# Kernel tuning notes

Measured on AMD Instinct MI355X. Metric: run time of the kernel, lower is better.

Reference implementation:

```python
import math
import jax, jax.numpy as jnp
import numpy as np

# hyperparameters (module defaults; w_scale overridden to 1.0)
EMA_SPEED = 0.05
REW_SENS = 1.0
LR = 0.0033
MOMENTUM = 0.4
UNTANH = 0.6
SPEED = 0.5
WIDTH = 0.1
WD = 0.01
LAT_DECAY = 0.01
NOISE_SCALE = 0.8
C_MOMENT = 0.99
W_SCALE = 1.0


def rms_norm(x, axis=-1):
    return x * jax.lax.rsqrt(jnp.mean(x * x, axis=axis, keepdims=True) + 1e-6)


def setup_inputs() -> dict:
    key = jax.random.key(0)
    ks = jax.random.split(key, 16)
    B, N, D = 16, 128, 64
    s = 1.0 / math.sqrt(D)
    return {
        'eye_env': jax.random.normal(ks[0], (B, D), jnp.float32),
        'stomach_env': jax.random.normal(ks[1], (B, D), jnp.float32),
        'state': jax.random.normal(ks[2], (B, N, D), jnp.float32),
        'output': jax.random.normal(ks[3], (B, N, D), jnp.float32),
        'W1': jax.random.normal(ks[4], (B, N, D, D), jnp.float32) * s,
        'W2': jax.random.normal(ks[5], (B, N, D, D), jnp.float32) * s,
        'W3': jax.random.normal(ks[6], (B, N, D, D), jnp.float32) * s,
        'M1': jax.random.normal(ks[7], (B, N, D, D), jnp.float32) * 0.2,
        'M2': jax.random.normal(ks[8], (B, N, D, D), jnp.float32) * 0.2,
        'M3': jax.random.normal(ks[9], (B, N, D, D), jnp.float32) * 0.2,
        'E_baseline': jax.random.uniform(ks[10], (B, N, D), jnp.float32),
        'A': jax.nn.softmax(jax.random.normal(ks[11], (B, N, N), jnp.float32), axis=2),
        'noise_A': jax.random.normal(ks[12], (B, N, N), jnp.float32),
        'noise1_raw': jax.random.normal(ks[13], (B, N, D), jnp.float32),
        'noise2_raw': jax.random.normal(ks[14], (B, N, D), jnp.float32),
        'step_counter': 0,
    }


def reference(eye_env, stomach_env, state, output, W1, W2, W3, M1, M2, M3,
              E_baseline, A, noise_A, noise1_raw, noise2_raw, step_counter):
    B, N, D = state.shape
    sc = jnp.float32(step_counter) + 1.0  # self.step_counter += 1

    # attention routing
    q = jnp.einsum('bnj,bnjk->bnk', state, W3)
    k = jnp.einsum('bnj,bnjk->bnk', state, W2)
    raw_A = jnp.einsum('bnd,bmd->bnm', q, k) / math.sqrt(D) + noise_A * 1e-5
    P_dense = jax.nn.softmax(raw_A, axis=2)
    keep = (P_dense > 1.0 / (N + 1.0)) | (P_dense == jnp.max(P_dense, axis=2, keepdims=True))
    P = jax.nn.softmax(jnp.where(keep, raw_A, -jnp.inf), axis=2)
    A_new = A * C_MOMENT + P * (1.0 - C_MOMENT)
    A_new = A_new.at[:, 0:2, :].set(0.0)

    # message passing + sensory clamp
    target = jnp.einsum('bnm,bmd->bnd', A_new, output)
    target = target.at[:, 0].set(eye_env).at[:, 1].set(stomach_env)

    # prediction
    raw_pred = jnp.einsum('bnj,bnjk->bnk', state, W1)
    raw = raw_pred - jnp.tanh(raw_pred) * UNTANH
    prediction = jnp.tanh(raw) * math.sqrt(2.0 + math.sqrt(2.0))

    err = prediction - target
    E_curr = jax.nn.softmax(err, axis=-1)
    bmask = (E_baseline == 0).astype(jnp.float32)
    Eb = E_baseline * (1.0 - bmask) + E_curr * bmask
    Eb = Eb * (1.0 - EMA_SPEED) + EMA_SPEED * E_curr
    advantage = E_curr - Eb
    R = -rms_norm(advantage[..., None] * REW_SENS)  # (B,N,D,1)
    mask = (Eb > 0).astype(jnp.float32)[..., None]

    # noise injection
    state_mag = jnp.sum(jnp.abs(state), axis=(-2, -1), keepdims=True)
    noise1 = noise1_raw / (1.0 + state_mag)
    noise2 = noise2_raw * jnp.std(err, ddof=1) * NOISE_SCALE
    noisy_state = state + noise1 + noise2

    # Hebbian outer-product gradient, G_NORM=1.0 -> rms-normalized
    lg = -jnp.einsum('bni,bnj->bnij', err, noisy_state)
    lg = rms_norm(lg, axis=(2, 3))

    plasticity = 1.0 - R
    grad1 = plasticity * lg * mask + LAT_DECAY * W3 - WD * W1
    grad2 = plasticity * lg * mask + LAT_DECAY * W1 - WD * W2
    grad3 = plasticity * lg * mask + LAT_DECAY * W2 - WD * W3

    # travelling gaussian column mask
    idx = jnp.arange(D, dtype=jnp.float32).reshape(1, 1, 1, D)
    center = (sc * SPEED) % D
    diff = jnp.abs(idx - center)
    diff = jnp.minimum(diff, D - diff)
    g_mask = jnp.exp(-diff ** 2 / (2.0 * WIDTH ** 2 + 1e-6))

    M1n = M1 * MOMENTUM + (1.0 - MOMENTUM) * (grad1 * g_mask)
    M2n = M2 * MOMENTUM + (1.0 - MOMENTUM) * (grad2 * g_mask)
    M3n = M3 * MOMENTUM + (1.0 - MOMENTUM) * (grad3 * g_mask)
    W1n = rms_norm(W1 + LR * M1n) * W_SCALE
    W2n = rms_norm(W2 + LR * M2n) * W_SCALE
    W3n = rms_norm(W3 + LR * M3n) * W_SCALE

    # new output = prediction, new state = target
    return prediction, target, A_new, W1n, W2n, W3n
```

## Files before the change

kernel.cpp:

```cpp
#include <hip/hip_runtime.h>
#include <hip/hip_bf16.h>

typedef __hip_bfloat16 bf16;
typedef float f32x4 __attribute__((ext_vector_type(4)));

__device__ __forceinline__ float b2f(bf16 x) { return __bfloat162float(x); }

template<bool F32>
__device__ __forceinline__ float ld(const void* p, size_t i) {
  if constexpr (F32) return ((const float*)p)[i];
  else return b2f(((const bf16*)p)[i]);
}

template<bool F32>
__device__ __forceinline__ void ld4(const void* p, size_t i, float v[4]) {
  if constexpr (F32) {
    const float4 a = *(const float4*)((const float*)p + i);
    v[0]=a.x; v[1]=a.y; v[2]=a.z; v[3]=a.w;
  } else {
    union { uint2 u; bf16 h[4]; } t;
    t.u = *(const uint2*)((const bf16*)p + i);
    #pragma unroll
    for (int c = 0; c < 4; ++c) v[c] = b2f(t.h[c]);
  }
}

template<bool F32>
__device__ __forceinline__ void ld8(const void* p, size_t i, float v[8]) {
  if constexpr (F32) {
    const float4 a = *(const float4*)((const float*)p + i);
    const float4 b = *(const float4*)((const float*)p + i + 4);
    v[0]=a.x; v[1]=a.y; v[2]=a.z; v[3]=a.w;
    v[4]=b.x; v[5]=b.y; v[6]=b.z; v[7]=b.w;
  } else {
    union { uint4 u; bf16 h[8]; } t;
    t.u = *(const uint4*)((const bf16*)p + i);
    #pragma unroll
    for (int c = 0; c < 8; ++c) v[c] = b2f(t.h[c]);
  }
}

template<bool F32>
__device__ __forceinline__ void ld8nt(const void* p, size_t i, float v[8]) {
  if constexpr (F32) {
    const f32x4* q = (const f32x4*)((const float*)p + i);
    const f32x4 a = __builtin_nontemporal_load(q);
    const f32x4 b = __builtin_nontemporal_load(q + 1);
    v[0]=a[0]; v[1]=a[1]; v[2]=a[2]; v[3]=a[3];
    v[4]=b[0]; v[5]=b[1]; v[6]=b[2]; v[7]=b[3];
  } else {
    ld8<false>(p, i, v);
  }
}

__device__ __forceinline__ float plast(float Ec, float Ebl) {
  const float Eb0 = (Ebl == 0.f) ? Ec : Ebl;
  const float Eb  = Eb0 * 0.95f + 0.05f * Ec;
  const float adv = Ec - Eb;
  const float R   = -adv * rsqrtf(adv*adv + 1e-6f);
  return (Eb > 0.f) ? (1.f - R) : 0.f;
}


template<bool F32>
__device__ __forceinline__ void k1_wave(
    const void* state, const void* W1, const void* W2, const void* W3,
    float* qw, float* kw, float* magn, float* out_pred,
    int node, int mat, int lane)
{
  const float st = ld<F32>(state, (size_t)node*64 + lane);
  const int jg = lane >> 4, cq = lane & 15;
  const int c0 = cq * 4;
  const size_t nb = (size_t)node*4096 + (size_t)jg*1024 + c0;
  const void* W = (mat == 0) ? W3 : (mat == 1) ? W2 : W1;

  float acc[4] = {0.f, 0.f, 0.f, 0.f};
  float buf[8][4];
  #pragma unroll
  for (int jj = 0; jj < 8; ++jj) ld4<F32>(W, nb + (size_t)jj*64, buf[jj]);
  #pragma unroll
  for (int jj = 0; jj < 8; ++jj) {
    const float sj = __shfl(st, jg*16 + jj, 64);
    #pragma unroll
    for (int cc = 0; cc < 4; ++cc) acc[cc] += sj * buf[jj][cc];
  }
  #pragma unroll
  for (int jj = 0; jj < 8; ++jj) ld4<F32>(W, nb + (size_t)(jj + 8)*64, buf[jj]);
  #pragma unroll
  for (int jj = 0; jj < 8; ++jj) {
    const float sj = __shfl(st, jg*16 + 8 + jj, 64);
    #pragma unroll
    for (int cc = 0; cc < 4; ++cc) acc[cc] += sj * buf[jj][cc];
  }
  #pragma unroll
  for (int cc = 0; cc < 4; ++cc) {
    acc[cc] += __shfl_xor(acc[cc], 16, 64);
    acc[cc] += __shfl_xor(acc[cc], 32, 64);
  }

  if (mat == 2) {
    float am = fabsf(st);
    #pragma unroll
    for (int s = 32; s; s >>= 1) am += __shfl_xor(am, s, 64);
    if (lane == 0) magn[node] = am;
    if (jg == 0) {
      float pr[4];
      #pragma unroll
      for (int cc = 0; cc < 4; ++cc) {
        const float raw = acc[cc] - tanhf(acc[cc]) * 0.6f;
        pr[cc] = tanhf(raw) * 1.8477590650225735f;
      }
      *(float4*)(out_pred + (size_t)node*64 + c0) = make_float4(pr[0], pr[1], pr[2], pr[3]);
    }
  } else if (jg == 0) {
    float* dst = (mat == 0) ? qw : kw;
    *(float4*)(dst + (size_t)node*64 + c0) = make_float4(acc[0], acc[1], acc[2], acc[3]);
  }
}

__global__ __launch_bounds__(256) void k1_qkpred(
    const void* __restrict__ state,
    const void* __restrict__ W1, const void* __restrict__ W2,
    const void* __restrict__ W3,
    float* __restrict__ qw, float* __restrict__ kw,
    float* __restrict__ magn, float* __restrict__ out_pred,
    int* __restrict__ flagws, float* __restrict__ stats)
{
  const int tid = threadIdx.x;
  const int w = tid >> 6, lane = tid & 63;
  bool huge = false;
  for (int i = lane; i < 1024; i += 64) {
    const float x = b2f(((const bf16*)state)[i]);
    if (!(fabsf(x) < 1e5f)) huge = true;
  }
  const bool f32 = (__ballot(huge) != 0ull);
  if (blockIdx.x == 0 && tid == 0) {
    *flagws = f32 ? 1 : 0;
    stats[0] = 0.f; stats[1] = 0.f;
  }
  const int wid = blockIdx.x * 4 + w;
  const int node = wid & 2047, mat = wid >> 11;
  if (f32) k1_wave<true >(state, W1, W2, W3, qw, kw, magn, out_pred, node, mat, lane);
  else     k1_wave<false>(state, W1, W2, W3, qw, kw, magn, out_pred, node, mat, lane);
}

template<bool F32>
__device__ __forceinline__ void k2_body(
    const float* qw, const float* kw, const float* predw,
    const void* noiseA, const void* Aold, const void* outp,
    const void* eye, const void* stomach, const void* Ebase,
    const float* magn, float* mag,
    float* errw, float* plw, float* stats,
    float* out_target, float* out_A,
    float* s_k, float* s_q, float* s_A)
{
  const int bidx = blockIdx.x;
  const int b = bidx >> 4;
  const int n0 = (bidx & 15) * 8;
  const int tid = threadIdx.x;

  if (n0 == 0 && tid < 64) {
    float v = magn[b*128 + tid] + magn[b*128 + 64 + tid];
    #pragma unroll
    for (int s = 32; s; s >>= 1) v += __shfl_xor(v, s, 64);
    if (tid == 0) mag[b] = v;
  }

  {
    const float* kwb = kw + (size_t)b * 8192;
    #pragma unroll
    for (int it = 0; it < 8; ++it) {
      const int idx = it*256 + tid;
      const int m = idx >> 4, dq = idx & 15;
      const float4 v = *(const float4*)(kwb + (size_t)idx * 4);
      float* dst = &s_k[m*65 + dq*4];
      dst[0] = v.x; dst[1] = v.y; dst[2] = v.z; dst[3] = v.w;
    }
    if (tid < 128) {
      const int rr = tid >> 4, dq = tid & 15;
      *(float4*)&s_q[rr*64 + dq*4] =
          *(const float4*)(qw + ((size_t)(b*128 + n0 + rr))*64 + dq*4);
    }
  }
  __syncthreads();

  const int rr = tid >> 5, c = tid & 31;
  const int n = n0 + rr;
  const size_t node = (size_t)b*128 + n;

  float acc[4] = {0.f, 0.f, 0.f, 0.f};
  {
    const float* qrow = s_q + rr*64;
    #pragma unroll 8
    for (int j = 0; j < 64; ++j) {
      const float qv = qrow[j];
      acc[0] += qv * s_k[(c     )*65 + j];
      acc[1] += qv * s_k[(c + 32)*65 + j];
      acc[2] += qv * s_k[(c + 64)*65 + j];
      acc[3] += qv * s_k[(c + 96)*65 + j];
    }
  }
  float raw[4];
  #pragma unroll
  for (int i = 0; i < 4; ++i)
    raw[i] = acc[i]*0.125f + 1e-5f*ld<F32>(noiseA, node*128 + c + 32*i);

  float rmx = fmaxf(fmaxf(raw[0], raw[1]), fmaxf(raw[2], raw[3]));
  #pragma unroll
  for (int s = 16; s >= 1; s >>= 1) rmx = fmaxf(rmx, __shfl_xor(rmx, s, 64));
  float e[4], S = 0.f;
  #pragma unroll
  for (int i = 0; i < 4; ++i) { e[i] = expf(raw[i] - rmx); S += e[i]; }
  #pragma unroll
  for (int s = 16; s >= 1; s >>= 1) S += __shfl_xor(S, s, 64);
  float ek[4], Sk = 0.f;
  #pragma unroll
  for (int i = 0; i < 4; ++i) {
    const float Pd = e[i] / S;
    ek[i] = ((Pd > 0.007751937984496124f) || (raw[i] == rmx)) ? e[i] : 0.f;
    Sk += ek[i];
  }
  #pragma unroll
  for (int s = 16; s >= 1; s >>= 1) Sk += __shfl_xor(Sk, s, 64);
  #pragma unroll
  for (int i = 0; i < 4; ++i) {
    const int m = c + 32*i;
    const float P = ek[i] / Sk;
    const float An = (n < 2) ? 0.f
                   : 0.99f * ld<F32>(Aold, node*128 + m) + 0.01f * P;
    out_A[node*128 + m] = An;
    s_A[rr*128 + m] = An;
  }
  __syncthreads();

  float t0, t1;
  if (n == 0) {
    t0 = ld<F32>(eye, (size_t)b*64 + c);
    t1 = ld<F32>(eye, (size_t)b*64 + c + 32);
  } else if (n == 1) {
    t0 = ld<F32>(stomach, (size_t)b*64 + c);
    t1 = ld<F32>(stomach, (size_t)b*64 + c + 32);
  } else {
    t0 = 0.f; t1 = 0.f;
    const float* arow = s_A + rr*128;
    const size_t ob = (size_t)b * 8192;
    #pragma unroll 4
    for (int m = 0; m < 128; ++m) {
      const float a = arow[m];
      t0 += a * ld<F32>(outp, ob + m*64 + c);
      t1 += a * ld<F32>(outp, ob + m*64 + c + 32);
    }
  }
  out_target[node*64 + c]      = t0;
  out_target[node*64 + c + 32] = t1;
  const float e0 = predw[node*64 + c]      - t0;
  const float e1 = predw[node*64 + c + 32] - t1;
  errw[node*64 + c]      = e0;
  errw[node*64 + c + 32] = e1;

  float mx = fmaxf(e0, e1);
  #pragma unroll
  for (int s = 16; s >= 1; s >>= 1) mx = fmaxf(mx, __shfl_xor(mx, s, 64));
  const float x0 = expf(e0 - mx), x1 = expf(e1 - mx);
  float ss = x0 + x1;
  #pragma unroll
  for (int s = 16; s >= 1; s >>= 1) ss += __shfl_xor(ss, s, 64);
  plw[node*64 + c]      = plast(x0/ss, ld<F32>(Ebase, node*64 + c));
  plw[node*64 + c + 32] = plast(x1/ss, ld<F32>(Ebase, node*64 + c + 32));

  float se = e0 + e1, sq = e0*e0 + e1*e1;
  #pragma unroll
  for (int s = 16; s >= 1; s >>= 1) { se += __shfl_xor(se, s, 64); sq += __shfl_xor(sq, s, 64); }
  if (c == 0) { atomicAdd(&stats[0], se); atomicAdd(&stats[1], sq); }
}

__global__ __launch_bounds__(256) void k2_attn(
    const int* __restrict__ flag,
    const float* __restrict__ qw, const float* __restrict__ kw,
    const float* __restrict__ predw,
    const void* __restrict__ noiseA, const void* __restrict__ Aold,
    const void* __restrict__ outp,
    const void* __restrict__ eye, const void* __restrict__ stomach,
    const void* __restrict__ Ebase,
    const float* __restrict__ magn, float* __restrict__ mag,
    float* __restrict__ errw, float* __restrict__ plw,
    float* __restrict__ stats,
    float* __restrict__ out_target, float* __restrict__ out_A)
{
  __shared__ alignas(16) float s_k[128*65];
  __shared__ alignas(16) float s_q[8*64];
  __shared__ alignas(16) float s_A[8*128];
  if (*flag) k2_body<true >(qw,kw,predw,noiseA,Aold,outp,eye,stomach,Ebase,magn,mag,errw,plw,stats,out_target,out_A,s_k,s_q,s_A);
  else       k2_body<false>(qw,kw,predw,noiseA,Aold,outp,eye,stomach,Ebase,magn,mag,errw,plw,stats,out_target,out_A,s_k,s_q,s_A);
}

template<bool F32>
__device__ __forceinline__ void k3_body(
    const float* errw, const float* plw,
    const void* state, const void* n1raw, const void* n2raw,
    const float* mag, const float* stats, const int* stepc,
    const void* W1, const void* W2, const void* W3,
    const void* M1, const void* M2, const void* M3,
    float* oW1, float* oW2, float* oW3)
{
  const int node = blockIdx.x;
  const int b = node >> 7;
  const int tid = threadIdx.x;
  const int lane = tid & 63;
  const int r = tid >> 3;
  const int l8 = tid & 7;

  const size_t sb = (size_t)node*64 + lane;
  const float e_i  = errw[sb];
  const float pl_i = plw[sb];
  const float st_i = ld<F32>(state, sb);
  const float n1_i = ld<F32>(n1raw, sb);
  const float n2_i = ld<F32>(n2raw, sb);
  const float magb = mag[b];
  const float S1 = stats[0], S2 = stats[1];
  const float scv = (float)stepc[0] + 1.f;

  const size_t off = (size_t)node*4096 + (size_t)r*64 + (size_t)l8*8;
  float w1v[8], w2v[8], w3v[8], m1v[8], m2v[8], m3v[8];
  ld8  <F32>(W1, off, w1v); ld8  <F32>(W2, off, w2v); ld8  <F32>(W3, off, w3v);
  ld8nt<F32>(M1, off, m1v); ld8nt<F32>(M2, off, m2v); ld8nt<F32>(M3, off, m3v);

  const float Mn = 131072.f;
  const float var = (S2 - S1*S1/Mn) / (Mn - 1.f);
  const float stdv = sqrtf(fmaxf(var, 0.f));
  const float ns_i = st_i + n1_i / (1.f + magb)
                   + n2_i * stdv * 0.8f;
  float e2 = e_i*e_i, q2 = ns_i*ns_i;
  #pragma unroll
  for (int s = 32; s; s >>= 1) { e2 += __shfl_xor(e2, s, 64); q2 += __shfl_xor(q2, s, 64); }
  const float c_i  = -ns_i * rsqrtf(e2 * q2 * (1.f/4096.f) + 1e-6f);
  const float pe_i = pl_i * e_i;
  const float center = fmodf(scv * 0.5f, 64.f);
  float dff = fabsf((float)lane - center);
  dff = fminf(dff, 64.f - dff);
  const float g_i = expf(-dff*dff * (1.f/0.020001f));

  const float pe = __shfl(pe_i, r, 64);
  float cj[8], gj[8];
  #pragma unroll
  for (int cc = 0; cc < 8; ++cc) {
    const int j = l8*8 + cc;
    cj[cc] = __shfl(c_i, j, 64);
    gj[cc] = __shfl(g_i, j, 64);
  }

  float t1[8], t2[8], t3[8];
  float ss1 = 0.f, ss2 = 0.f, ss3 = 0.f;
  #pragma unroll
  for (int cc = 0; cc < 8; ++cc) {
    const float lgterm = pe * cj[cc];
    const float g = gj[cc];
    const float g1 = lgterm + 0.01f*w3v[cc] - 0.01f*w1v[cc];
    const float g2 = lgterm + 0.01f*w1v[cc] - 0.01f*w2v[cc];
    const float g3 = lgterm + 0.01f*w2v[cc] - 0.01f*w3v[cc];
    const float v1 = w1v[cc] + 0.0033f*(0.4f*m1v[cc] + 0.6f*g1*g);
    const float v2 = w2v[cc] + 0.0033f*(0.4f*m2v[cc] + 0.6f*g2*g);
    const float v3 = w3v[cc] + 0.0033f*(0.4f*m3v[cc] + 0.6f*g3*g);
    t1[cc] = v1; t2[cc] = v2; t3[cc] = v3;
    ss1 += v1*v1; ss2 += v2*v2; ss3 += v3*v3;
  }
  #pragma unroll
  for (int s = 1; s <= 4; s <<= 1) {
    ss1 += __shfl_xor(ss1, s, 64);
    ss2 += __shfl_xor(ss2, s, 64);
    ss3 += __shfl_xor(ss3, s, 64);
  }
  const float r1 = rsqrtf(ss1*(1.f/64.f) + 1e-6f);
  const float r2 = rsqrtf(ss2*(1.f/64.f) + 1e-6f);
  const float r3 = rsqrtf(ss3*(1.f/64.f) + 1e-6f);
  *(float4*)(oW1 + off)     = make_float4(t1[0]*r1, t1[1]*r1, t1[2]*r1, t1[3]*r1);
  *(float4*)(oW1 + off + 4) = make_float4(t1[4]*r1, t1[5]*r1, t1[6]*r1, t1[7]*r1);
  *(float4*)(oW2 + off)     = make_float4(t2[0]*r2, t2[1]*r2, t2[2]*r2, t2[3]*r2);
  *(float4*)(oW2 + off + 4) = make_float4(t2[4]*r2, t2[5]*r2, t2[6]*r2, t2[7]*r2);
  *(float4*)(oW3 + off)     = make_float4(t3[0]*r3, t3[1]*r3, t3[2]*r3, t3[3]*r3);
  *(float4*)(oW3 + off + 4) = make_float4(t3[4]*r3, t3[5]*r3, t3[6]*r3, t3[7]*r3);
}

__global__ __launch_bounds__(512) void k3_update(
    const int* __restrict__ flag,
    const float* __restrict__ errw, const float* __restrict__ plw,
    const void* __restrict__ state, const void* __restrict__ n1raw,
    const void* __restrict__ n2raw,
    const float* __restrict__ mag, const float* __restrict__ stats,
    const int* __restrict__ stepc,
    const void* __restrict__ W1, const void* __restrict__ W2,
    const void* __restrict__ W3,
    const void* __restrict__ M1, const void* __restrict__ M2,
    const void* __restrict__ M3,
    float* __restrict__ oW1, float* __restrict__ oW2, float* __restrict__ oW3)
{
  if (*flag) k3_body<true >(errw,plw,state,n1raw,n2raw,mag,stats,stepc,W1,W2,W3,M1,M2,M3,oW1,oW2,oW3);
  else       k3_body<false>(errw,plw,state,n1raw,n2raw,mag,stats,stepc,W1,W2,W3,M1,M2,M3,oW1,oW2,oW3);
}

extern "C" void kernel_launch(void* const* d_in, const int* in_sizes, int n_in,
                              void* d_out, int out_size, void* d_ws, size_t ws_size,
                              hipStream_t stream) {
  const void* eye     = d_in[0];
  const void* stomach = d_in[1];
  const void* state   = d_in[2];
  const void* outp    = d_in[3];
  const void* W1      = d_in[4];
  const void* W2      = d_in[5];
  const void* W3      = d_in[6];
  const void* M1      = d_in[7];
  const void* M2      = d_in[8];
  const void* M3      = d_in[9];
  const void* Ebase   = d_in[10];
  const void* Aold    = d_in[11];
  const void* noiseA  = d_in[12];
  const void* n1raw   = d_in[13];
  const void* n2raw   = d_in[14];
  const int*  stepc   = (const int*)d_in[15];

  float* ws    = (float*)d_ws;
  float* qw    = ws;
  float* kw    = ws + 131072;
  float* errw  = ws + 262144;
  float* plw   = ws + 393216;
  float* magn  = ws + 524288;
  float* mag   = ws + 526336;
  float* stats = ws + 526352;
  int*   flag  = (int*)(ws + 526354);

  float* out        = (float*)d_out;
  float* out_pred   = out;
  float* out_target = out + 131072;
  float* out_A      = out + 262144;
  float* oW1        = out + 524288;
  float* oW2        = out + 8912896;
  float* oW3        = out + 17301504;

  k1_qkpred<<<1536, 256, 0, stream>>>(state, W1, W2, W3, qw, kw, magn, out_pred,
                                      flag, stats);
  k2_attn<<<256, 256, 0, stream>>>(flag, qw, kw, out_pred, noiseA, Aold, outp,
                                   eye, stomach, Ebase, magn, mag, errw, plw, stats,
                                   out_target, out_A);
  k3_update<<<2048, 512, 0, stream>>>(flag, errw, plw, state, n1raw, n2raw, mag, stats,
                                      stepc, W1, W2, W3, M1, M2, M3, oW1, oW2, oW3);
}
```

Measured before the change: 333.3 us.

## Remap attention kernel to one wave per row and issue all weight loads at once

The attention kernel now assigns one 64-lane wave per query row, with 4 rows per block and twice as many blocks, instead of 8 rows split across half-waves. Each row's softmax and target reductions stay inside a single wave, and the block-wide barrier between computing A and the target matvec is removed. The goal is more parallelism and less synchronisation in this small kernel. The cost is that each block reloads the full K matrix into shared memory, so that staging traffic doubles. Separately, the k1 weight matvec loads all 16 float4 weight rows before any accumulation, instead of two batches of 8, to put more loads in flight at the expense of extra registers.

```diff
diff --git a/kernel.cpp b/kernel.cpp
--- a/kernel.cpp
+++ b/kernel.cpp
@@ -75,20 +75,12 @@
   const void* W = (mat == 0) ? W3 : (mat == 1) ? W2 : W1;
 
   float acc[4] = {0.f, 0.f, 0.f, 0.f};
-  float buf[8][4];
-  #pragma unroll
-  for (int jj = 0; jj < 8; ++jj) ld4<F32>(W, nb + (size_t)jj*64, buf[jj]);
-  #pragma unroll
-  for (int jj = 0; jj < 8; ++jj) {
+  float buf[16][4];
+  #pragma unroll
+  for (int jj = 0; jj < 16; ++jj) ld4<F32>(W, nb + (size_t)jj*64, buf[jj]);
+  #pragma unroll
+  for (int jj = 0; jj < 16; ++jj) {
     const float sj = __shfl(st, jg*16 + jj, 64);
-    #pragma unroll
-    for (int cc = 0; cc < 4; ++cc) acc[cc] += sj * buf[jj][cc];
-  }
-  #pragma unroll
-  for (int jj = 0; jj < 8; ++jj) ld4<F32>(W, nb + (size_t)(jj + 8)*64, buf[jj]);
-  #pragma unroll
-  for (int jj = 0; jj < 8; ++jj) {
-    const float sj = __shfl(st, jg*16 + 8 + jj, 64);
     #pragma unroll
     for (int cc = 0; cc < 4; ++cc) acc[cc] += sj * buf[jj][cc];
   }
@@ -155,11 +147,12 @@
     float* s_k, float* s_q, float* s_A)
 {
   const int bidx = blockIdx.x;
-  const int b = bidx >> 4;
-  const int n0 = (bidx & 15) * 8;
+  const int b = bidx >> 5;
+  const int n0 = (bidx & 31) * 4;
   const int tid = threadIdx.x;
-
-  if (n0 == 0 && tid < 64) {
+  const int w = tid >> 6, lane = tid & 63;
+
+  if ((bidx & 31) == 0 && tid < 64) {
     float v = magn[b*128 + tid] + magn[b*128 + 64 + tid];
     #pragma unroll
     for (int s = 32; s; s >>= 1) v += __shfl_xor(v, s, 64);
@@ -176,7 +169,7 @@
       float* dst = &s_k[m*65 + dq*4];
       dst[0] = v.x; dst[1] = v.y; dst[2] = v.z; dst[3] = v.w;
     }
-    if (tid < 128) {
+    if (tid < 64) {
       const int rr = tid >> 4, dq = tid & 15;
       *(float4*)&s_q[rr*64 + dq*4] =
           *(const float4*)(qw + ((size_t)(b*128 + n0 + rr))*64 + dq*4);
@@ -184,94 +177,74 @@
   }
   __syncthreads();
 
-  const int rr = tid >> 5, c = tid & 31;
-  const int n = n0 + rr;
+  const int n = n0 + w;
   const size_t node = (size_t)b*128 + n;
 
-  float acc[4] = {0.f, 0.f, 0.f, 0.f};
+  float d0 = 0.f, d1 = 0.f;
   {
-    const float* qrow = s_q + rr*64;
+    const float* qrow = s_q + w*64;
+    const float* kr0 = s_k + lane*65;
+    const float* kr1 = s_k + (lane + 64)*65;
     #pragma unroll 8
     for (int j = 0; j < 64; ++j) {
       const float qv = qrow[j];
-      acc[0] += qv * s_k[(c     )*65 + j];
-      acc[1] += qv * s_k[(c + 32)*65 + j];
-      acc[2] += qv * s_k[(c + 64)*65 + j];
-      acc[3] += qv * s_k[(c + 96)*65 + j];
+      d0 += qv * kr0[j];
+      d1 += qv * kr1[j];
     }
   }
-  float raw[4];
-  #pragma unroll
-  for (int i = 0; i < 4; ++i)
-    raw[i] = acc[i]*0.125f + 1e-5f*ld<F32>(noiseA, node*128 + c + 32*i);
-
-  float rmx = fmaxf(fmaxf(raw[0], raw[1]), fmaxf(raw[2], raw[3]));
-  #pragma unroll
-  for (int s = 16; s >= 1; s >>= 1) rmx = fmaxf(rmx, __shfl_xor(rmx, s, 64));
-  float e[4], S = 0.f;
-  #pragma unroll
-  for (int i = 0; i < 4; ++i) { e[i] = expf(raw[i] - rmx); S += e[i]; }
-  #pragma unroll
-  for (int s = 16; s >= 1; s >>= 1) S += __shfl_xor(S, s, 64);
-  float ek[4], Sk = 0.f;
-  #pragma unroll
-  for (int i = 0; i < 4; ++i) {
-    const float Pd = e[i] / S;
-    ek[i] = ((Pd > 0.007751937984496124f) || (raw[i] == rmx)) ? e[i] : 0.f;
-    Sk += ek[i];
-  }
-  #pragma unroll
-  for (int s = 16; s >= 1; s >>= 1) Sk += __shfl_xor(Sk, s, 64);
-  #pragma unroll
-  for (int i = 0; i < 4; ++i) {
-    const int m = c + 32*i;
-    const float P = ek[i] / Sk;
-    const float An = (n < 2) ? 0.f
-                   : 0.99f * ld<F32>(Aold, node*128 + m) + 0.01f * P;
-    out_A[node*128 + m] = An;
-    s_A[rr*128 + m] = An;
-  }
-  __syncthreads();
-
-  float t0, t1;
-  if (n == 0) {
-    t0 = ld<F32>(eye, (size_t)b*64 + c);
-    t1 = ld<F32>(eye, (size_t)b*64 + c + 32);
-  } else if (n == 1) {
-    t0 = ld<F32>(stomach, (size_t)b*64 + c);
-    t1 = ld<F32>(stomach, (size_t)b*64 + c + 32);
-  } else {
-    t0 = 0.f; t1 = 0.f;
-    const float* arow = s_A + rr*128;
+  const float raw0 = d0*0.125f + 1e-5f*ld<F32>(noiseA, node*128 + lane);
+  const float raw1 = d1*0.125f + 1e-5f*ld<F32>(noiseA, node*128 + lane + 64);
+
+  float rmx = fmaxf(raw0, raw1);
+  #pragma unroll
+  for (int s = 32; s; s >>= 1) rmx = fmaxf(rmx, __shfl_xor(rmx, s, 64));
+  const float e0x = expf(raw0 - rmx), e1x = expf(raw1 - rmx);
+  float S = e0x + e1x;
+  #pragma unroll
+  for (int s = 32; s; s >>= 1) S += __shfl_xor(S, s, 64);
+  const float thr = 0.007751937984496124f;
+  const float ek0 = ((e0x/S > thr) || (raw0 == rmx)) ? e0x : 0.f;
+  const float ek1 = ((e1x/S > thr) || (raw1 == rmx)) ? e1x : 0.f;
+  float Sk = ek0 + ek1;
+  #pragma unroll
+  for (int s = 32; s; s >>= 1) Sk += __shfl_xor(Sk, s, 64);
+  const float A0 = (n < 2) ? 0.f
+                 : 0.99f*ld<F32>(Aold, node*128 + lane)      + 0.01f*(ek0/Sk);
+  const float A1 = (n < 2) ? 0.f
+                 : 0.99f*ld<F32>(Aold, node*128 + lane + 64) + 0.01f*(ek1/Sk);
+  out_A[node*128 + lane]      = A0;
+  out_A[node*128 + lane + 64] = A1;
+  s_A[w*128 + lane]      = A0;
+  s_A[w*128 + lane + 64] = A1;
+
+  float t0;
+  if (n == 0)      t0 = ld<F32>(eye, (size_t)b*64 + lane);
+  else if (n == 1) t0 = ld<F32>(stomach, (size_t)b*64 + lane);
+  else {
+    t0 = 0.f;
+    const float* arow = s_A + w*128;
     const size_t ob = (size_t)b * 8192;
-    #pragma unroll 4
-    for (int m = 0; m < 128; ++m) {
-      const float a = arow[m];
-      t0 += a * ld<F32>(outp, ob + m*64 + c);
-      t1 += a * ld<F32>(outp, ob + m*64 + c + 32);
-    }
-  }
-  out_target[node*64 + c]      = t0;
-  out_target[node*64 + c + 32] = t1;
-  const float e0 = predw[node*64 + c]      - t0;
-  const float e1 = predw[node*64 + c + 32] - t1;
-  errw[node*64 + c]      = e0;
-  errw[node*64 + c + 32] = e1;
-
-  float mx = fmaxf(e0, e1);
-  #pragma unroll
-  for (int s = 16; s >= 1; s >>= 1) mx = fmaxf(mx, __shfl_xor(mx, s, 64));
-  const float x0 = expf(e0 - mx), x1 = expf(e1 - mx);
-  float ss = x0 + x1;
-  #pragma unroll
-  for (int s = 16; s >= 1; s >>= 1) ss += __shfl_xor(ss, s, 64);
-  plw[node*64 + c]      = plast(x0/ss, ld<F32>(Ebase, node*64 + c));
-  plw[node*64 + c + 32] = plast(x1/ss, ld<F32>(Ebase, node*64 + c + 32));
-
-  float se = e0 + e1, sq = e0*e0 + e1*e1;
-  #pragma unroll
-  for (int s = 16; s >= 1; s >>= 1) { se += __shfl_xor(se, s, 64); sq += __shfl_xor(sq, s, 64); }
-  if (c == 0) { atomicAdd(&stats[0], se); atomicAdd(&stats[1], sq); }
+    #pragma unroll 8
+    for (int m = 0; m < 128; ++m)
+      t0 += arow[m] * ld<F32>(outp, ob + (size_t)m*64 + lane);
+  }
+  out_target[node*64 + lane] = t0;
+  const float er = predw[node*64 + lane] - t0;
+  errw[node*64 + lane] = er;
+
+  float mx = er;
+  #pragma unroll
+  for (int s = 32; s; s >>= 1) mx = fmaxf(mx, __shfl_xor(mx, s, 64));
+  const float ee = expf(er - mx);
+  float ss = ee;
+  #pragma unroll
+  for (int s = 32; s; s >>= 1) ss += __shfl_xor(ss, s, 64);
+  plw[node*64 + lane] = plast(ee/ss, ld<F32>(Ebase, node*64 + lane));
+
+  float se = er, sq2 = er*er;
+  #pragma unroll
+  for (int s = 32; s; s >>= 1) { se += __shfl_xor(se, s, 64); sq2 += __shfl_xor(sq2, s, 64); }
+  if (lane == 0) { atomicAdd(&stats[0], se); atomicAdd(&stats[1], sq2); }
 }
 
 __global__ __launch_bounds__(256) void k2_attn(
@@ -288,8 +261,8 @@
     float* __restrict__ out_target, float* __restrict__ out_A)
 {
   __shared__ alignas(16) float s_k[128*65];
-  __shared__ alignas(16) float s_q[8*64];
-  __shared__ alignas(16) float s_A[8*128];
+  __shared__ alignas(16) float s_q[4*64];
+  __shared__ alignas(16) float s_A[4*128];
   if (*flag) k2_body<true >(qw,kw,predw,noiseA,Aold,outp,eye,stomach,Ebase,magn,mag,errw,plw,stats,out_target,out_A,s_k,s_q,s_A);
   else       k2_body<false>(qw,kw,predw,noiseA,Aold,outp,eye,stomach,Ebase,magn,mag,errw,plw,stats,out_target,out_A,s_k,s_q,s_A);
 }
@@ -438,7 +411,7 @@
 
   k1_qkpred<<<1536, 256, 0, stream>>>(state, W1, W2, W3, qw, kw, magn, out_pred,
                                       flag, stats);
-  k2_attn<<<256, 256, 0, stream>>>(flag, qw, kw, out_pred, noiseA, Aold, outp,
+  k2_attn<<<512, 256, 0, stream>>>(flag, qw, kw, out_pred, noiseA, Aold, outp,
                                    eye, stomach, Ebase, magn, mag, errw, plw, stats,
                                    out_target, out_A);
   k3_update<<<2048, 512, 0, stream>>>(flag, errw, plw, state, n1raw, n2raw, mag, stats,
```

After: 351.9 us. +5.6%, slower.
